# Optimization experiments

Hardware: AMD Instinct MI355X
Metric: run time of the kernel (lower is better)

The kernel has to match this reference:

```python
import jax, jax.numpy as jnp
import numpy as np

B, T, D, H = 2, 2048, 1024, 16
DH = D // H  # 64


def setup_inputs() -> dict:
    key = jax.random.key(0)
    ks = jax.random.split(key, 6)
    s = 1.0 / np.sqrt(D)
    return {
        "x": jax.random.normal(ks[0], (B, T, D), dtype=jnp.float32),
        "Wq": jax.random.normal(ks[1], (D, D), dtype=jnp.float32) * s,
        "Wk": jax.random.normal(ks[2], (D, D), dtype=jnp.float32) * s,
        "Wv": jax.random.normal(ks[3], (D, D), dtype=jnp.float32) * s,
        "Wo": jax.random.normal(ks[4], (D, D), dtype=jnp.float32) * s,
        "bo": jnp.zeros((D,), dtype=jnp.float32),
    }


def reference(x, Wq, Wk, Wv, Wo, bo):
    b, t, _ = x.shape
    # projections (torch Linear: x @ W.T; here W stored as [d_in, d_out])
    q = (x @ Wq).reshape(b, t, H, DH).transpose(0, 2, 1, 3)  # [b,H,t,dh]
    k = (x @ Wk).reshape(b, t, H, DH).transpose(0, 2, 1, 3)
    v = (x @ Wv).reshape(b, t, H, DH).transpose(0, 2, 1, 3)
    scores = jnp.einsum("bhqd,bhkd->bhqk", q, k) / np.sqrt(DH).astype(np.float32)
    causal = jnp.tril(jnp.ones((t, t), dtype=bool))  # True = keep
    scores = jnp.where(causal, scores, -jnp.inf)
    weights = jax.nn.softmax(scores, axis=-1)
    ctx = jnp.einsum("bhqk,bhkd->bhqd", weights, v)
    ctx = ctx.transpose(0, 2, 1, 3).reshape(b, t, D)
    return ctx @ Wo + bo
```

## Files before the change

kernel.cpp:

```cpp
#include <hip/hip_runtime.h>


typedef unsigned short u16;
typedef __attribute__((ext_vector_type(8))) short short8;
typedef __attribute__((ext_vector_type(4))) short short4_t;
typedef __attribute__((ext_vector_type(4))) float f32x4;

#define B_ 2
#define T_ 2048
#define D_ 1024
#define H_ 16
#define DH_ 64
#define M_ (B_ * T_)
#define SCALE_LOG2E 0.18033688011112042f
#define NEG_BIG -3.0e4f

#define SLOT_F 4160
#define SLOTS_PER_BH 72
#define OPART_BYTES ((size_t)32 * SLOTS_PER_BH * SLOT_F * 4)
#define WS_BASE_BYTES ((size_t)24 * 1024 * 1024 * 2)

#define GLOAD16(g, l)                                                     \
  __builtin_amdgcn_global_load_lds(                                       \
      (const __attribute__((address_space(1))) void*)(g),                 \
      (__attribute__((address_space(3))) void*)(l), 16, 0, 0)

__device__ __forceinline__ u16 f2bf(float f) {
  union { float f; unsigned u; } v; v.f = f;
  unsigned r = v.u + 0x7fffu + ((v.u >> 16) & 1u);
  return (u16)(r >> 16);
}
__device__ __forceinline__ u16 f2bf_trunc(float f) {
  union { float f; unsigned u; } v; v.f = f;
  return (u16)(v.u >> 16);
}
__device__ __forceinline__ float exp2_raw(float x) {
  float r;
  asm volatile("v_exp_f32 %0, %1" : "=v"(r) : "v"(x));
  return r;
}

__global__ __launch_bounds__(256) void cvt_x(const float* __restrict__ x,
                                             u16* __restrict__ xb) {
  const int i = (blockIdx.x * 256 + threadIdx.x) * 8;
  float4 a = *(const float4*)(x + i);
  float4 b = *(const float4*)(x + i + 4);
  short8 o;
  o[0] = (short)f2bf(a.x); o[1] = (short)f2bf(a.y);
  o[2] = (short)f2bf(a.z); o[3] = (short)f2bf(a.w);
  o[4] = (short)f2bf(b.x); o[5] = (short)f2bf(b.y);
  o[6] = (short)f2bf(b.z); o[7] = (short)f2bf(b.w);
  *(short8*)(xb + i) = o;
}

__global__ __launch_bounds__(256) void transpose_w(
    const float* __restrict__ w0, const float* __restrict__ w1,
    const float* __restrict__ w2, const float* __restrict__ w3,
    u16* __restrict__ outT) {
  __shared__ u16 Tl[64][72];
  const int z = blockIdx.z;
  const float* src = (z == 0) ? w0 : (z == 1) ? w1 : (z == 2) ? w2 : w3;
  const int r0 = blockIdx.y * 64, c0 = blockIdx.x * 64;
  const int tid = threadIdx.x;
  const int rr = tid >> 2, cc = (tid & 3) * 16;

  const float* p = src + (size_t)(r0 + rr) * D_ + c0 + cc;
  float4 f0 = *(const float4*)p;
  float4 f1 = *(const float4*)(p + 4);
  float4 f2 = *(const float4*)(p + 8);
  float4 f3 = *(const float4*)(p + 12);
  Tl[rr][cc + 0] = f2bf(f0.x); Tl[rr][cc + 1] = f2bf(f0.y);
  Tl[rr][cc + 2] = f2bf(f0.z); Tl[rr][cc + 3] = f2bf(f0.w);
  Tl[rr][cc + 4] = f2bf(f1.x); Tl[rr][cc + 5] = f2bf(f1.y);
  Tl[rr][cc + 6] = f2bf(f1.z); Tl[rr][cc + 7] = f2bf(f1.w);
  Tl[rr][cc + 8] = f2bf(f2.x); Tl[rr][cc + 9] = f2bf(f2.y);
  Tl[rr][cc +10] = f2bf(f2.z); Tl[rr][cc +11] = f2bf(f2.w);
  Tl[rr][cc +12] = f2bf(f3.x); Tl[rr][cc +13] = f2bf(f3.y);
  Tl[rr][cc +14] = f2bf(f3.z); Tl[rr][cc +15] = f2bf(f3.w);
  __syncthreads();

  u16* o = outT + (size_t)z * D_ * D_ + (size_t)(c0 + rr) * D_ + r0 + cc;
  short8 x0, x1;
#pragma unroll
  for (int i = 0; i < 8; i++) x0[i] = (short)Tl[cc + i][rr];
#pragma unroll
  for (int i = 0; i < 8; i++) x1[i] = (short)Tl[cc + 8 + i][rr];
  *(short8*)o = x0;
  *(short8*)(o + 8) = x1;
}

__global__ __launch_bounds__(256) void qkv_gemm(
    const u16* __restrict__ x, const u16* __restrict__ wT,
    u16* __restrict__ qkv) {
  __shared__ u16 As[128][32];
  __shared__ u16 Bs[128][32];

  const int z = blockIdx.z;
  const u16* W = wT + (size_t)z * D_ * D_;
  u16* out = qkv + (size_t)z * M_ * D_;
  const int n0 = blockIdx.x * 128;
  const int m0 = blockIdx.y * 128;
  const int tid = threadIdx.x;
  const int lane = tid & 63, w = tid >> 6;
  const int quad = lane >> 4, l16 = lane & 15;
  const int wr = w >> 1, wc = w & 1;

  f32x4 acc[4][4] = {};
  const int grow = w * 16 + (lane >> 2);
  const int gcol = (lane & 3) * 8;
  u16* lA = (u16*)As + w * 512;
  u16* lB = (u16*)Bs + w * 512;

  for (int k0 = 0; k0 < D_; k0 += 32) {
    const u16* gA = x + (size_t)(m0 + grow) * D_ + k0 + gcol;
    const u16* gB = W + (size_t)(n0 + grow) * D_ + k0 + gcol;
    GLOAD16(gA, lA);
    GLOAD16(gA + (size_t)64 * D_, lA + 2048);
    GLOAD16(gB, lB);
    GLOAD16(gB + (size_t)64 * D_, lB + 2048);
    __syncthreads();

    short8 af[4], bf[4];
#pragma unroll
    for (int i = 0; i < 4; i++)
      af[i] = *(const short8*)&As[wr * 64 + i * 16 + l16][quad * 8];
#pragma unroll
    for (int i = 0; i < 4; i++)
      bf[i] = *(const short8*)&Bs[wc * 64 + i * 16 + l16][quad * 8];
#pragma unroll
    for (int i = 0; i < 4; i++)
#pragma unroll
      for (int j = 0; j < 4; j++)
        acc[i][j] = __builtin_amdgcn_mfma_f32_16x16x32_bf16(af[i], bf[j], acc[i][j], 0, 0, 0);
    __syncthreads();
  }

  const float osc = (z == 0) ? SCALE_LOG2E : 1.0f;
#pragma unroll
  for (int i = 0; i < 4; i++) {
#pragma unroll
    for (int j = 0; j < 4; j++) {
      const int n = n0 + wc * 64 + j * 16 + l16;
      const int h = n >> 6, dh = n & 63;
#pragma unroll
      for (int r = 0; r < 4; r++) {
        const int m = m0 + wr * 64 + i * 16 + quad * 4 + r;
        const int b = m >> 11, t = m & (T_ - 1);
        out[(((size_t)(b * H_ + h)) * T_ + t) * DH_ + dh] = f2bf(acc[i][j][r] * osc);
      }
    }
  }
}

__global__ __launch_bounds__(256) void transpose_v(
    const u16* __restrict__ v, u16* __restrict__ vT) {
  __shared__ u16 Tl[64][72];
  const int t0 = blockIdx.x * 64;
  const int bh = blockIdx.y;
  const int tid = threadIdx.x;
  const int rr = tid >> 2, cc = (tid & 3) * 16;

  const u16* p = v + (size_t)bh * T_ * DH_ + (size_t)(t0 + rr) * DH_ + cc;
  short8 a0 = *(const short8*)p;
  short8 a1 = *(const short8*)(p + 8);
  *(short8*)&Tl[rr][cc] = a0;
  *(short8*)&Tl[rr][cc + 8] = a1;
  __syncthreads();

  u16* o = vT + (size_t)bh * DH_ * T_ + (size_t)rr * T_ + t0 + cc;
  short8 x0, x1;
#pragma unroll
  for (int i = 0; i < 8; i++) x0[i] = (short)Tl[cc + i][rr];
#pragma unroll
  for (int i = 0; i < 8; i++) x1[i] = (short)Tl[cc + 8 + i][rr];
  *(short8*)o = x0;
  *(short8*)(o + 8) = x1;
}

__device__ __forceinline__ int slot_base(int qt) {
  return (qt < 16) ? (qt - 8) * 2
       : (qt < 24) ? 16 + (qt - 16) * 3
                   : 40 + (qt - 24) * 4;
}

__global__ __launch_bounds__(128) void attn_chunk(
    const u16* __restrict__ qg, const u16* __restrict__ kg,
    const u16* __restrict__ vtg, u16* __restrict__ ctx,
    float* __restrict__ Opart) {
  __shared__ u16 Ks[64][72];
  __shared__ u16 Vs[64][72];
  __shared__ u16 Ps[2][2][16][72];

  const int cid = 79 - blockIdx.x;
  int qt, c, nc;
  if (cid < 8)       { qt = cid;                    c = 0;               nc = 1; }
  else if (cid < 24) { qt = 8  + ((cid - 8) >> 1);  c = (cid - 8) & 1;   nc = 2; }
  else if (cid < 48) { qt = 16 + (cid - 24) / 3;    c = (cid - 24) % 3;  nc = 3; }
  else               { qt = 24 + ((cid - 48) >> 2); c = (cid - 48) & 3;  nc = 4; }
  const int nt = qt + 1;
  const int kv_lo = (c * nt / nc) * 64;
  const int kv_hi = ((c + 1) * nt / nc) * 64;
  const int q0 = qt * 64;

  const int bh = blockIdx.y;
  const int tid = threadIdx.x;
  const int w = tid >> 6, lane = tid & 63;
  const int quad = lane >> 4, l16 = lane & 15;
  const size_t baseQK = (size_t)bh * T_ * DH_;
  const size_t baseV  = (size_t)bh * DH_ * T_;

  const int qrowA = q0 + w * 32 + l16;
  const int qrowB = qrowA + 16;
  short8 qfA0 = *(const short8*)(qg + baseQK + (size_t)qrowA * DH_ + quad * 8);
  short8 qfA1 = *(const short8*)(qg + baseQK + (size_t)qrowA * DH_ + 32 + quad * 8);
  short8 qfB0 = *(const short8*)(qg + baseQK + (size_t)qrowB * DH_ + quad * 8);
  short8 qfB1 = *(const short8*)(qg + baseQK + (size_t)qrowB * DH_ + 32 + quad * 8);

  f32x4 oaccA[4] = {}, oaccB[4] = {};
  float liA = 0.f, liB = 0.f;

  const int srow = tid >> 1;
  const int scol = (tid & 1) * 32;

  const u16* kp = kg + baseQK + (size_t)(kv_lo + srow) * DH_ + scol;
  const u16* vp = vtg + baseV + (size_t)srow * T_ + kv_lo + scol;
  short8 kr0 = *(const short8*)kp;
  short8 kr1 = *(const short8*)(kp + 8);
  short8 kr2 = *(const short8*)(kp + 16);
  short8 kr3 = *(const short8*)(kp + 24);
  short8 vr0 = *(const short8*)vp;
  short8 vr1 = *(const short8*)(vp + 8);
  short8 vr2 = *(const short8*)(vp + 16);
  short8 vr3 = *(const short8*)(vp + 24);

  for (int kv0 = kv_lo; kv0 < kv_hi; kv0 += 64) {
    __syncthreads();
    *(short8*)&Ks[srow][scol]      = kr0;
    *(short8*)&Ks[srow][scol + 8]  = kr1;
    *(short8*)&Ks[srow][scol + 16] = kr2;
    *(short8*)&Ks[srow][scol + 24] = kr3;
    *(short8*)&Vs[srow][scol]      = vr0;
    *(short8*)&Vs[srow][scol + 8]  = vr1;
    *(short8*)&Vs[srow][scol + 16] = vr2;
    *(short8*)&Vs[srow][scol + 24] = vr3;
    if (kv0 + 64 < kv_hi) {
      const u16* kn = kg + baseQK + (size_t)(kv0 + 64 + srow) * DH_ + scol;
      const u16* vn = vtg + baseV + (size_t)srow * T_ + kv0 + 64 + scol;
      kr0 = *(const short8*)kn;
      kr1 = *(const short8*)(kn + 8);
      kr2 = *(const short8*)(kn + 16);
      kr3 = *(const short8*)(kn + 24);
      vr0 = *(const short8*)vn;
      vr1 = *(const short8*)(vn + 8);
      vr2 = *(const short8*)(vn + 16);
      vr3 = *(const short8*)(vn + 24);
    }
    __syncthreads();

    short8 kf0[4], kf1[4];
#pragma unroll
    for (int cb = 0; cb < 4; cb++) {
      kf0[cb] = *(const short8*)&Ks[cb * 16 + l16][quad * 8];
      kf1[cb] = *(const short8*)&Ks[cb * 16 + l16][32 + quad * 8];
    }

    f32x4 svA[4], svB[4];
    __builtin_amdgcn_s_setprio(1);
#pragma unroll
    for (int cb = 0; cb < 4; cb++) {
      f32x4 z = {};
      svA[cb] = __builtin_amdgcn_mfma_f32_16x16x32_bf16(kf0[cb], qfA0, z, 0, 0, 0);
      svA[cb] = __builtin_amdgcn_mfma_f32_16x16x32_bf16(kf1[cb], qfA1, svA[cb], 0, 0, 0);
      svB[cb] = __builtin_amdgcn_mfma_f32_16x16x32_bf16(kf0[cb], qfB0, z, 0, 0, 0);
      svB[cb] = __builtin_amdgcn_mfma_f32_16x16x32_bf16(kf1[cb], qfB1, svB[cb], 0, 0, 0);
    }
    __builtin_amdgcn_s_setprio(0);

    float pA[4][4], pB[4][4];
    if (kv0 == q0) {
#pragma unroll
      for (int cb = 0; cb < 4; cb++)
#pragma unroll
        for (int r = 0; r < 4; r++) {
          const int kv = kv0 + cb * 16 + quad * 4 + r;
          pA[cb][r] = exp2_raw((kv <= qrowA) ? svA[cb][r] : NEG_BIG);
          pB[cb][r] = exp2_raw((kv <= qrowB) ? svB[cb][r] : NEG_BIG);
        }
    } else {
#pragma unroll
      for (int cb = 0; cb < 4; cb++)
#pragma unroll
        for (int r = 0; r < 4; r++) {
          pA[cb][r] = exp2_raw(svA[cb][r]);
          pB[cb][r] = exp2_raw(svB[cb][r]);
        }
    }
#pragma unroll
    for (int cb = 0; cb < 4; cb++)
#pragma unroll
      for (int r = 0; r < 4; r++) { liA += pA[cb][r]; liB += pB[cb][r]; }

    short8 vf0[4], vf1[4];
#pragma unroll
    for (int cb = 0; cb < 4; cb++) {
      vf0[cb] = *(const short8*)&Vs[cb * 16 + l16][quad * 8];
      vf1[cb] = *(const short8*)&Vs[cb * 16 + l16][32 + quad * 8];
    }

#pragma unroll
    for (int cb = 0; cb < 4; cb++) {
      short4_t pkA, pkB;
#pragma unroll
      for (int r = 0; r < 4; r++) {
        pkA[r] = (short)f2bf_trunc(pA[cb][r]);
        pkB[r] = (short)f2bf_trunc(pB[cb][r]);
      }
      *(short4_t*)&Ps[w][0][l16][cb * 16 + quad * 4] = pkA;
      *(short4_t*)&Ps[w][1][l16][cb * 16 + quad * 4] = pkB;
    }
    short8 paA0 = *(const short8*)&Ps[w][0][l16][quad * 8];
    short8 paA1 = *(const short8*)&Ps[w][0][l16][32 + quad * 8];
    short8 paB0 = *(const short8*)&Ps[w][1][l16][quad * 8];
    short8 paB1 = *(const short8*)&Ps[w][1][l16][32 + quad * 8];
    __builtin_amdgcn_s_setprio(1);
#pragma unroll
    for (int cb = 0; cb < 4; cb++) {
      oaccA[cb] = __builtin_amdgcn_mfma_f32_16x16x32_bf16(vf0[cb], paA0, oaccA[cb], 0, 0, 0);
      oaccA[cb] = __builtin_amdgcn_mfma_f32_16x16x32_bf16(vf1[cb], paA1, oaccA[cb], 0, 0, 0);
      oaccB[cb] = __builtin_amdgcn_mfma_f32_16x16x32_bf16(vf0[cb], paB0, oaccB[cb], 0, 0, 0);
      oaccB[cb] = __builtin_amdgcn_mfma_f32_16x16x32_bf16(vf1[cb], paB1, oaccB[cb], 0, 0, 0);
    }
    __builtin_amdgcn_s_setprio(0);
  }

  liA += __shfl_xor(liA, 16, 64); liA += __shfl_xor(liA, 32, 64);
  liB += __shfl_xor(liB, 16, 64); liB += __shfl_xor(liB, 32, 64);

  if (nc == 1) {
    const int b = bh >> 4, h = bh & 15;
    const float invA = 1.0f / liA, invB = 1.0f / liB;
    u16* outA = ctx + ((size_t)(b * T_ + qrowA)) * D_ + h * 64 + quad * 4;
    u16* outB = ctx + ((size_t)(b * T_ + qrowB)) * D_ + h * 64 + quad * 4;
#pragma unroll
    for (int cb = 0; cb < 4; cb++) {
      short4_t oA, oB;
#pragma unroll
      for (int r = 0; r < 4; r++) {
        oA[r] = (short)f2bf(oaccA[cb][r] * invA);
        oB[r] = (short)f2bf(oaccB[cb][r] * invB);
      }
      *(short4_t*)(outA + cb * 16) = oA;
      *(short4_t*)(outB + cb * 16) = oB;
    }
  } else {
    float* slot = Opart + ((size_t)bh * SLOTS_PER_BH + slot_base(qt) + c) * SLOT_F;
    float* pA = slot + (size_t)(w * 32 + l16) * 64 + quad * 4;
    float* pB = slot + (size_t)(w * 32 + 16 + l16) * 64 + quad * 4;
#pragma unroll
    for (int cb = 0; cb < 4; cb++) {
      *(f32x4*)(pA + cb * 16) = oaccA[cb];
      *(f32x4*)(pB + cb * 16) = oaccB[cb];
    }
    if (quad == 0) {
      slot[4096 + w * 32 + l16] = liA;
      slot[4096 + w * 32 + 16 + l16] = liB;
    }
  }
}

__global__ __launch_bounds__(256) void attn_combine(
    const float* __restrict__ Opart, u16* __restrict__ ctx) {
  __shared__ float ls[64];
  const int qt = blockIdx.x + 8;
  const int bh = blockIdx.y;
  const int nc = 1 + (qt >> 3);
  const float* slot0 = Opart + ((size_t)bh * SLOTS_PER_BH + slot_base(qt)) * SLOT_F;
  const int tid = threadIdx.x;

  if (tid < 64) {
    float s = 0.f;
    for (int c = 0; c < nc; c++) s += slot0[(size_t)c * SLOT_F + 4096 + tid];
    ls[tid] = 1.0f / s;
  }
  __syncthreads();

  const int q = tid >> 2, d0 = (tid & 3) * 16;
  const float* p = slot0 + (size_t)q * 64 + d0;
  f32x4 a0 = *(const f32x4*)(p);
  f32x4 a1 = *(const f32x4*)(p + 4);
  f32x4 a2 = *(const f32x4*)(p + 8);
  f32x4 a3 = *(const f32x4*)(p + 12);
  for (int c = 1; c < nc; c++) {
    const float* pc = p + (size_t)c * SLOT_F;
    a0 += *(const f32x4*)(pc);
    a1 += *(const f32x4*)(pc + 4);
    a2 += *(const f32x4*)(pc + 8);
    a3 += *(const f32x4*)(pc + 12);
  }
  const float inv = ls[q];
  short8 o0, o1;
#pragma unroll
  for (int i = 0; i < 4; i++) {
    o0[i]     = (short)f2bf(a0[i] * inv);
    o0[i + 4] = (short)f2bf(a1[i] * inv);
    o1[i]     = (short)f2bf(a2[i] * inv);
    o1[i + 4] = (short)f2bf(a3[i] * inv);
  }
  const int b = bh >> 4, h = bh & 15;
  u16* op = ctx + ((size_t)(b * T_ + qt * 64 + q)) * D_ + h * 64 + d0;
  *(short8*)op = o0;
  *(short8*)(op + 8) = o1;
}

__global__ __launch_bounds__(128) void attn_mono(
    const u16* __restrict__ qg, const u16* __restrict__ kg,
    const u16* __restrict__ vtg, u16* __restrict__ ctx) {
  __shared__ u16 Ks[64][72];
  __shared__ u16 Vs[64][72];
  __shared__ u16 Ps[2][2][16][72];

  const int qt = gridDim.x - 1 - blockIdx.x;
  const int bh = blockIdx.y;
  const int tid = threadIdx.x;
  const int w = tid >> 6, lane = tid & 63;
  const int quad = lane >> 4, l16 = lane & 15;
  const int q0 = qt * 64;
  const size_t baseQK = (size_t)bh * T_ * DH_;
  const size_t baseV  = (size_t)bh * DH_ * T_;

  const int qrowA = q0 + w * 32 + l16;
  const int qrowB = qrowA + 16;
  short8 qfA0 = *(const short8*)(qg + baseQK + (size_t)qrowA * DH_ + quad * 8);
  short8 qfA1 = *(const short8*)(qg + baseQK + (size_t)qrowA * DH_ + 32 + quad * 8);
  short8 qfB0 = *(const short8*)(qg + baseQK + (size_t)qrowB * DH_ + quad * 8);
  short8 qfB1 = *(const short8*)(qg + baseQK + (size_t)qrowB * DH_ + 32 + quad * 8);

  f32x4 oaccA[4] = {}, oaccB[4] = {};
  float liA = 0.f, liB = 0.f;

  const int srow = tid >> 1;
  const int scol = (tid & 1) * 32;

  const u16* kp = kg + baseQK + (size_t)srow * DH_ + scol;
  const u16* vp = vtg + baseV + (size_t)srow * T_ + scol;
  short8 kr0 = *(const short8*)kp;
  short8 kr1 = *(const short8*)(kp + 8);
  short8 kr2 = *(const short8*)(kp + 16);
  short8 kr3 = *(const short8*)(kp + 24);
  short8 vr0 = *(const short8*)vp;
  short8 vr1 = *(const short8*)(vp + 8);
  short8 vr2 = *(const short8*)(vp + 16);
  short8 vr3 = *(const short8*)(vp + 24);

  for (int kv0 = 0; kv0 <= q0; kv0 += 64) {
    __syncthreads();
    *(short8*)&Ks[srow][scol]      = kr0;
    *(short8*)&Ks[srow][scol + 8]  = kr1;
    *(short8*)&Ks[srow][scol + 16] = kr2;
    *(short8*)&Ks[srow][scol + 24] = kr3;
    *(short8*)&Vs[srow][scol]      = vr0;
    *(short8*)&Vs[srow][scol + 8]  = vr1;
    *(short8*)&Vs[srow][scol + 16] = vr2;
    *(short8*)&Vs[srow][scol + 24] = vr3;
    if (kv0 < q0) {
      const u16* kn = kg + baseQK + (size_t)(kv0 + 64 + srow) * DH_ + scol;
      const u16* vn = vtg + baseV + (size_t)srow * T_ + kv0 + 64 + scol;
      kr0 = *(const short8*)kn;
      kr1 = *(const short8*)(kn + 8);
      kr2 = *(const short8*)(kn + 16);
      kr3 = *(const short8*)(kn + 24);
      vr0 = *(const short8*)vn;
      vr1 = *(const short8*)(vn + 8);
      vr2 = *(const short8*)(vn + 16);
      vr3 = *(const short8*)(vn + 24);
    }
    __syncthreads();

    short8 kf0[4], kf1[4];
#pragma unroll
    for (int cb = 0; cb < 4; cb++) {
      kf0[cb] = *(const short8*)&Ks[cb * 16 + l16][quad * 8];
      kf1[cb] = *(const short8*)&Ks[cb * 16 + l16][32 + quad * 8];
    }

    f32x4 svA[4], svB[4];
#pragma unroll
    for (int cb = 0; cb < 4; cb++) {
      f32x4 z = {};
      svA[cb] = __builtin_amdgcn_mfma_f32_16x16x32_bf16(kf0[cb], qfA0, z, 0, 0, 0);
      svA[cb] = __builtin_amdgcn_mfma_f32_16x16x32_bf16(kf1[cb], qfA1, svA[cb], 0, 0, 0);
      svB[cb] = __builtin_amdgcn_mfma_f32_16x16x32_bf16(kf0[cb], qfB0, z, 0, 0, 0);
      svB[cb] = __builtin_amdgcn_mfma_f32_16x16x32_bf16(kf1[cb], qfB1, svB[cb], 0, 0, 0);
    }

    float pA[4][4], pB[4][4];
    if (kv0 == q0) {
#pragma unroll
      for (int cb = 0; cb < 4; cb++)
#pragma unroll
        for (int r = 0; r < 4; r++) {
          const int kv = kv0 + cb * 16 + quad * 4 + r;
          pA[cb][r] = exp2_raw((kv <= qrowA) ? svA[cb][r] : NEG_BIG);
          pB[cb][r] = exp2_raw((kv <= qrowB) ? svB[cb][r] : NEG_BIG);
        }
    } else {
#pragma unroll
      for (int cb = 0; cb < 4; cb++)
#pragma unroll
        for (int r = 0; r < 4; r++) {
          pA[cb][r] = exp2_raw(svA[cb][r]);
          pB[cb][r] = exp2_raw(svB[cb][r]);
        }
    }
#pragma unroll
    for (int cb = 0; cb < 4; cb++)
#pragma unroll
      for (int r = 0; r < 4; r++) { liA += pA[cb][r]; liB += pB[cb][r]; }

    short8 vf0[4], vf1[4];
#pragma unroll
    for (int cb = 0; cb < 4; cb++) {
      vf0[cb] = *(const short8*)&Vs[cb * 16 + l16][quad * 8];
      vf1[cb] = *(const short8*)&Vs[cb * 16 + l16][32 + quad * 8];
    }

#pragma unroll
    for (int cb = 0; cb < 4; cb++) {
      short4_t pkA, pkB;
#pragma unroll
      for (int r = 0; r < 4; r++) {
        pkA[r] = (short)f2bf_trunc(pA[cb][r]);
        pkB[r] = (short)f2bf_trunc(pB[cb][r]);
      }
      *(short4_t*)&Ps[w][0][l16][cb * 16 + quad * 4] = pkA;
      *(short4_t*)&Ps[w][1][l16][cb * 16 + quad * 4] = pkB;
    }
    short8 paA0 = *(const short8*)&Ps[w][0][l16][quad * 8];
    short8 paA1 = *(const short8*)&Ps[w][0][l16][32 + quad * 8];
    short8 paB0 = *(const short8*)&Ps[w][1][l16][quad * 8];
    short8 paB1 = *(const short8*)&Ps[w][1][l16][32 + quad * 8];
#pragma unroll
    for (int cb = 0; cb < 4; cb++) {
      oaccA[cb] = __builtin_amdgcn_mfma_f32_16x16x32_bf16(vf0[cb], paA0, oaccA[cb], 0, 0, 0);
      oaccA[cb] = __builtin_amdgcn_mfma_f32_16x16x32_bf16(vf1[cb], paA1, oaccA[cb], 0, 0, 0);
      oaccB[cb] = __builtin_amdgcn_mfma_f32_16x16x32_bf16(vf0[cb], paB0, oaccB[cb], 0, 0, 0);
      oaccB[cb] = __builtin_amdgcn_mfma_f32_16x16x32_bf16(vf1[cb], paB1, oaccB[cb], 0, 0, 0);
    }
  }

  liA += __shfl_xor(liA, 16, 64); liA += __shfl_xor(liA, 32, 64);
  liB += __shfl_xor(liB, 16, 64); liB += __shfl_xor(liB, 32, 64);
  const int b = bh >> 4, h = bh & 15;
  const float invA = 1.0f / liA, invB = 1.0f / liB;
  u16* outA = ctx + ((size_t)(b * T_ + qrowA)) * D_ + h * 64 + quad * 4;
  u16* outB = ctx + ((size_t)(b * T_ + qrowB)) * D_ + h * 64 + quad * 4;
#pragma unroll
  for (int cb = 0; cb < 4; cb++) {
    short4_t oA, oB;
#pragma unroll
    for (int r = 0; r < 4; r++) {
      oA[r] = (short)f2bf(oaccA[cb][r] * invA);
      oB[r] = (short)f2bf(oaccB[cb][r] * invB);
    }
    *(short4_t*)(outA + cb * 16) = oA;
    *(short4_t*)(outB + cb * 16) = oB;
  }
}

__global__ __launch_bounds__(256) void out_gemm(
    const u16* __restrict__ ctx, const u16* __restrict__ woT,
    const float* __restrict__ bo, float* __restrict__ out) {
  __shared__ u16 As[64][32];
  __shared__ u16 Bs[128][32];

  const int n0 = blockIdx.x * 128;
  const int m0 = blockIdx.y * 64;
  const int tid = threadIdx.x;
  const int lane = tid & 63, w = tid >> 6;
  const int quad = lane >> 4, l16 = lane & 15;
  const int wr = w >> 1, wc = w & 1;

  f32x4 acc[2][4] = {};
  const int grow = w * 16 + (lane >> 2);
  const int gcol = (lane & 3) * 8;
  u16* lA = (u16*)As + w * 512;
  u16* lB = (u16*)Bs + w * 512;

  for (int k0 = 0; k0 < D_; k0 += 32) {
    const u16* gA = ctx + (size_t)(m0 + grow) * D_ + k0 + gcol;
    const u16* gB = woT + (size_t)(n0 + grow) * D_ + k0 + gcol;
    GLOAD16(gA, lA);
    GLOAD16(gB, lB);
    GLOAD16(gB + (size_t)64 * D_, lB + 2048);
    __syncthreads();

    short8 af[2], bf[4];
#pragma unroll
    for (int i = 0; i < 2; i++)
      af[i] = *(const short8*)&As[wr * 32 + i * 16 + l16][quad * 8];
#pragma unroll
    for (int i = 0; i < 4; i++)
      bf[i] = *(const short8*)&Bs[wc * 64 + i * 16 + l16][quad * 8];
#pragma unroll
    for (int i = 0; i < 2; i++)
#pragma unroll
      for (int j = 0; j < 4; j++)
        acc[i][j] = __builtin_amdgcn_mfma_f32_16x16x32_bf16(af[i], bf[j], acc[i][j], 0, 0, 0);
    __syncthreads();
  }

#pragma unroll
  for (int i = 0; i < 2; i++) {
#pragma unroll
    for (int j = 0; j < 4; j++) {
      const int n = n0 + wc * 64 + j * 16 + l16;
      const float bias = bo[n];
#pragma unroll
      for (int r = 0; r < 4; r++) {
        const int m = m0 + wr * 32 + i * 16 + quad * 4 + r;
        out[(size_t)m * D_ + n] = acc[i][j][r] + bias;
      }
    }
  }
}

extern "C" void kernel_launch(void* const* d_in, const int* in_sizes, int n_in,
                              void* d_out, int out_size, void* d_ws, size_t ws_size,
                              hipStream_t stream) {
  const float* x  = (const float*)d_in[0];
  const float* Wq = (const float*)d_in[1];
  const float* Wk = (const float*)d_in[2];
  const float* Wv = (const float*)d_in[3];
  const float* Wo = (const float*)d_in[4];
  const float* bo = (const float*)d_in[5];
  float* out = (float*)d_out;

  u16* ws  = (u16*)d_ws;
  u16* xb  = ws;
  u16* wT  = xb + (size_t)M_ * D_;
  u16* qkv = wT + (size_t)4 * D_ * D_;
  u16* ctx = qkv + (size_t)3 * M_ * D_;
  u16* vT  = xb;
  float* Opart = (float*)(ctx + (size_t)M_ * D_);

  cvt_x<<<dim3(M_ * D_ / (256 * 8)), 256, 0, stream>>>(x, xb);
  transpose_w<<<dim3(16, 16, 4), 256, 0, stream>>>(Wq, Wk, Wv, Wo, wT);
  qkv_gemm<<<dim3(D_ / 128, M_ / 128, 3), 256, 0, stream>>>(xb, wT, qkv);
  transpose_v<<<dim3(T_ / 64, B_ * H_), 256, 0, stream>>>(qkv + (size_t)2 * M_ * D_, vT);

  if (ws_size >= WS_BASE_BYTES + OPART_BYTES) {
    attn_chunk<<<dim3(80, B_ * H_), 128, 0, stream>>>(
        qkv, qkv + (size_t)M_ * D_, vT, ctx, Opart);
    attn_combine<<<dim3(24, B_ * H_), 256, 0, stream>>>(Opart, ctx);
  } else {
    attn_mono<<<dim3(T_ / 64, B_ * H_), 128, 0, stream>>>(
        qkv, qkv + (size_t)M_ * D_, vT, ctx);
  }

  out_gemm<<<dim3(D_ / 128, M_ / 64), 256, 0, stream>>>(ctx, wT + (size_t)3 * D_ * D_, bo, out);
}
```

Before: 198.1 us.

## Load K/V MFMA fragments directly from global memory, dropping LDS staging

The attention kernel no longer stages K and V tiles in shared memory behind two barriers per iteration. Each wave now loads its MFMA operand fragments straight from global memory (served by L2/L1, since both waves read the same data), and the launch bounds request 4 blocks per SIMD. This removes the LDS write/read traffic and the block-wide syncs, and the lower LDS footprint may allow more blocks per CU. The cost is duplicated global loads across the two waves and no register prefetch of the next tile, so latency is exposed unless occupancy hides it.

```diff
diff --git a/kernel.cpp b/kernel.cpp
--- a/kernel.cpp
+++ b/kernel.cpp
@@ -183,12 +183,10 @@
                    : 40 + (qt - 24) * 4;
 }
 
-__global__ __launch_bounds__(128) void attn_chunk(
+__global__ __launch_bounds__(128, 4) void attn_chunk(
     const u16* __restrict__ qg, const u16* __restrict__ kg,
     const u16* __restrict__ vtg, u16* __restrict__ ctx,
     float* __restrict__ Opart) {
-  __shared__ u16 Ks[64][72];
-  __shared__ u16 Vs[64][72];
   __shared__ u16 Ps[2][2][16][72];
 
   const int cid = 79 - blockIdx.x;
@@ -219,49 +217,22 @@
   f32x4 oaccA[4] = {}, oaccB[4] = {};
   float liA = 0.f, liB = 0.f;
 
-  const int srow = tid >> 1;
-  const int scol = (tid & 1) * 32;
-
-  const u16* kp = kg + baseQK + (size_t)(kv_lo + srow) * DH_ + scol;
-  const u16* vp = vtg + baseV + (size_t)srow * T_ + kv_lo + scol;
-  short8 kr0 = *(const short8*)kp;
-  short8 kr1 = *(const short8*)(kp + 8);
-  short8 kr2 = *(const short8*)(kp + 16);
-  short8 kr3 = *(const short8*)(kp + 24);
-  short8 vr0 = *(const short8*)vp;
-  short8 vr1 = *(const short8*)(vp + 8);
-  short8 vr2 = *(const short8*)(vp + 16);
-  short8 vr3 = *(const short8*)(vp + 24);
+  const u16* kRow = kg + baseQK + (size_t)l16 * DH_ + quad * 8;
+  const u16* vRow = vtg + baseV + (size_t)l16 * T_ + quad * 8;
 
   for (int kv0 = kv_lo; kv0 < kv_hi; kv0 += 64) {
-    __syncthreads();
-    *(short8*)&Ks[srow][scol]      = kr0;
-    *(short8*)&Ks[srow][scol + 8]  = kr1;
-    *(short8*)&Ks[srow][scol + 16] = kr2;
-    *(short8*)&Ks[srow][scol + 24] = kr3;
-    *(short8*)&Vs[srow][scol]      = vr0;
-    *(short8*)&Vs[srow][scol + 8]  = vr1;
-    *(short8*)&Vs[srow][scol + 16] = vr2;
-    *(short8*)&Vs[srow][scol + 24] = vr3;
-    if (kv0 + 64 < kv_hi) {
-      const u16* kn = kg + baseQK + (size_t)(kv0 + 64 + srow) * DH_ + scol;
-      const u16* vn = vtg + baseV + (size_t)srow * T_ + kv0 + 64 + scol;
-      kr0 = *(const short8*)kn;
-      kr1 = *(const short8*)(kn + 8);
-      kr2 = *(const short8*)(kn + 16);
-      kr3 = *(const short8*)(kn + 24);
-      vr0 = *(const short8*)vn;
-      vr1 = *(const short8*)(vn + 8);
-      vr2 = *(const short8*)(vn + 16);
-      vr3 = *(const short8*)(vn + 24);
-    }
-    __syncthreads();
-
-    short8 kf0[4], kf1[4];
-#pragma unroll
-    for (int cb = 0; cb < 4; cb++) {
-      kf0[cb] = *(const short8*)&Ks[cb * 16 + l16][quad * 8];
-      kf1[cb] = *(const short8*)&Ks[cb * 16 + l16][32 + quad * 8];
+    short8 kf0[4], kf1[4], vf0[4], vf1[4];
+#pragma unroll
+    for (int cb = 0; cb < 4; cb++) {
+      const u16* kp = kRow + (size_t)(kv0 + cb * 16) * DH_;
+      kf0[cb] = *(const short8*)kp;
+      kf1[cb] = *(const short8*)(kp + 32);
+    }
+#pragma unroll
+    for (int cb = 0; cb < 4; cb++) {
+      const u16* vp = vRow + (size_t)(cb * 16) * T_ + kv0;
+      vf0[cb] = *(const short8*)vp;
+      vf1[cb] = *(const short8*)(vp + 32);
     }
 
     f32x4 svA[4], svB[4];
@@ -299,13 +270,6 @@
     for (int cb = 0; cb < 4; cb++)
 #pragma unroll
       for (int r = 0; r < 4; r++) { liA += pA[cb][r]; liB += pB[cb][r]; }
-
-    short8 vf0[4], vf1[4];
-#pragma unroll
-    for (int cb = 0; cb < 4; cb++) {
-      vf0[cb] = *(const short8*)&Vs[cb * 16 + l16][quad * 8];
-      vf1[cb] = *(const short8*)&Vs[cb * 16 + l16][32 + quad * 8];
-    }
 
 #pragma unroll
     for (int cb = 0; cb < 4; cb++) {
```

After: 281.8 us. 42.3% more time.

## Widen attention chunk query tile to 128 rows with four waves per block

Applied to the files above, without the earlier changes.

Each attention chunk block now covers a 128-row query tile using four waves (256 threads) instead of 64 rows with two waves. Every K/V tile loaded into LDS is therefore reused by twice as many query rows, which halves K/V global traffic and the number of blocks, and the KV split table, slot layout and combine kernel are resized to match. The causal mask now applies per wave whenever a KV tile overlaps that wave's rows. In exchange the grid has half as many blocks (1280), so there is less parallelism and coarser load balancing, and some waves compute fully masked tiles on the diagonal.

```diff
diff --git a/kernel.cpp b/kernel.cpp
--- a/kernel.cpp
+++ b/kernel.cpp
@@ -15,8 +15,8 @@
 #define SCALE_LOG2E 0.18033688011112042f
 #define NEG_BIG -3.0e4f
 
-#define SLOT_F 4160
-#define SLOTS_PER_BH 72
+#define SLOT_F 8320
+#define SLOTS_PER_BH 36
 #define OPART_BYTES ((size_t)32 * SLOTS_PER_BH * SLOT_F * 4)
 #define WS_BASE_BYTES ((size_t)24 * 1024 * 1024 * 2)
 
@@ -178,29 +178,29 @@
 }
 
 __device__ __forceinline__ int slot_base(int qt) {
-  return (qt < 16) ? (qt - 8) * 2
-       : (qt < 24) ? 16 + (qt - 16) * 3
-                   : 40 + (qt - 24) * 4;
-}
-
-__global__ __launch_bounds__(128) void attn_chunk(
+  return (qt < 8)  ? (qt - 4) * 2
+       : (qt < 12) ? 8 + (qt - 8) * 3
+                   : 20 + (qt - 12) * 4;
+}
+
+__global__ __launch_bounds__(256) void attn_chunk(
     const u16* __restrict__ qg, const u16* __restrict__ kg,
     const u16* __restrict__ vtg, u16* __restrict__ ctx,
     float* __restrict__ Opart) {
   __shared__ u16 Ks[64][72];
   __shared__ u16 Vs[64][72];
-  __shared__ u16 Ps[2][2][16][72];
-
-  const int cid = 79 - blockIdx.x;
+  __shared__ u16 Ps[4][2][16][72];
+
+  const int cid = 39 - blockIdx.x;
   int qt, c, nc;
-  if (cid < 8)       { qt = cid;                    c = 0;               nc = 1; }
-  else if (cid < 24) { qt = 8  + ((cid - 8) >> 1);  c = (cid - 8) & 1;   nc = 2; }
-  else if (cid < 48) { qt = 16 + (cid - 24) / 3;    c = (cid - 24) % 3;  nc = 3; }
-  else               { qt = 24 + ((cid - 48) >> 2); c = (cid - 48) & 3;  nc = 4; }
-  const int nt = qt + 1;
+  if (cid < 4)       { qt = cid;                    c = 0;               nc = 1; }
+  else if (cid < 12) { qt = 4  + ((cid - 4) >> 1);  c = (cid - 4) & 1;   nc = 2; }
+  else if (cid < 24) { qt = 8  + (cid - 12) / 3;    c = (cid - 12) % 3;  nc = 3; }
+  else               { qt = 12 + ((cid - 24) >> 2); c = (cid - 24) & 3;  nc = 4; }
+  const int nt = 2 * (qt + 1);
   const int kv_lo = (c * nt / nc) * 64;
   const int kv_hi = ((c + 1) * nt / nc) * 64;
-  const int q0 = qt * 64;
+  const int q0 = qt * 128;
 
   const int bh = blockIdx.y;
   const int tid = threadIdx.x;
@@ -209,7 +209,8 @@
   const size_t baseQK = (size_t)bh * T_ * DH_;
   const size_t baseV  = (size_t)bh * DH_ * T_;
 
-  const int qrowA = q0 + w * 32 + l16;
+  const int qw0 = q0 + w * 32;
+  const int qrowA = qw0 + l16;
   const int qrowB = qrowA + 16;
   short8 qfA0 = *(const short8*)(qg + baseQK + (size_t)qrowA * DH_ + quad * 8);
   short8 qfA1 = *(const short8*)(qg + baseQK + (size_t)qrowA * DH_ + 32 + quad * 8);
@@ -219,41 +220,29 @@
   f32x4 oaccA[4] = {}, oaccB[4] = {};
   float liA = 0.f, liB = 0.f;
 
-  const int srow = tid >> 1;
-  const int scol = (tid & 1) * 32;
+  const int srow = tid >> 2;
+  const int scol = (tid & 3) * 16;
 
   const u16* kp = kg + baseQK + (size_t)(kv_lo + srow) * DH_ + scol;
   const u16* vp = vtg + baseV + (size_t)srow * T_ + kv_lo + scol;
   short8 kr0 = *(const short8*)kp;
   short8 kr1 = *(const short8*)(kp + 8);
-  short8 kr2 = *(const short8*)(kp + 16);
-  short8 kr3 = *(const short8*)(kp + 24);
   short8 vr0 = *(const short8*)vp;
   short8 vr1 = *(const short8*)(vp + 8);
-  short8 vr2 = *(const short8*)(vp + 16);
-  short8 vr3 = *(const short8*)(vp + 24);
 
   for (int kv0 = kv_lo; kv0 < kv_hi; kv0 += 64) {
     __syncthreads();
-    *(short8*)&Ks[srow][scol]      = kr0;
-    *(short8*)&Ks[srow][scol + 8]  = kr1;
-    *(short8*)&Ks[srow][scol + 16] = kr2;
-    *(short8*)&Ks[srow][scol + 24] = kr3;
-    *(short8*)&Vs[srow][scol]      = vr0;
-    *(short8*)&Vs[srow][scol + 8]  = vr1;
-    *(short8*)&Vs[srow][scol + 16] = vr2;
-    *(short8*)&Vs[srow][scol + 24] = vr3;
+    *(short8*)&Ks[srow][scol]     = kr0;
+    *(short8*)&Ks[srow][scol + 8] = kr1;
+    *(short8*)&Vs[srow][scol]     = vr0;
+    *(short8*)&Vs[srow][scol + 8] = vr1;
     if (kv0 + 64 < kv_hi) {
       const u16* kn = kg + baseQK + (size_t)(kv0 + 64 + srow) * DH_ + scol;
       const u16* vn = vtg + baseV + (size_t)srow * T_ + kv0 + 64 + scol;
       kr0 = *(const short8*)kn;
       kr1 = *(const short8*)(kn + 8);
-      kr2 = *(const short8*)(kn + 16);
-      kr3 = *(const short8*)(kn + 24);
       vr0 = *(const short8*)vn;
       vr1 = *(const short8*)(vn + 8);
-      vr2 = *(const short8*)(vn + 16);
-      vr3 = *(const short8*)(vn + 24);
     }
     __syncthreads();
 
@@ -277,7 +266,7 @@
     __builtin_amdgcn_s_setprio(0);
 
     float pA[4][4], pB[4][4];
-    if (kv0 == q0) {
+    if (kv0 + 63 > qw0) {
 #pragma unroll
       for (int cb = 0; cb < 4; cb++)
 #pragma unroll
@@ -362,54 +351,68 @@
       *(f32x4*)(pB + cb * 16) = oaccB[cb];
     }
     if (quad == 0) {
-      slot[4096 + w * 32 + l16] = liA;
-      slot[4096 + w * 32 + 16 + l16] = liB;
+      slot[8192 + w * 32 + l16] = liA;
+      slot[8192 + w * 32 + 16 + l16] = liB;
     }
   }
 }
 
 __global__ __launch_bounds__(256) void attn_combine(
     const float* __restrict__ Opart, u16* __restrict__ ctx) {
-  __shared__ float ls[64];
-  const int qt = blockIdx.x + 8;
+  __shared__ float ls[128];
+  const int qt = blockIdx.x + 4;
   const int bh = blockIdx.y;
-  const int nc = 1 + (qt >> 3);
+  const int nc = 1 + (qt >> 2);
   const float* slot0 = Opart + ((size_t)bh * SLOTS_PER_BH + slot_base(qt)) * SLOT_F;
   const int tid = threadIdx.x;
 
-  if (tid < 64) {
+  if (tid < 128) {
     float s = 0.f;
-    for (int c = 0; c < nc; c++) s += slot0[(size_t)c * SLOT_F + 4096 + tid];
+    for (int c = 0; c < nc; c++) s += slot0[(size_t)c * SLOT_F + 8192 + tid];
     ls[tid] = 1.0f / s;
   }
   __syncthreads();
 
-  const int q = tid >> 2, d0 = (tid & 3) * 16;
+  const int q = tid >> 1, d0 = (tid & 1) * 32;
   const float* p = slot0 + (size_t)q * 64 + d0;
   f32x4 a0 = *(const f32x4*)(p);
   f32x4 a1 = *(const f32x4*)(p + 4);
   f32x4 a2 = *(const f32x4*)(p + 8);
   f32x4 a3 = *(const f32x4*)(p + 12);
+  f32x4 a4 = *(const f32x4*)(p + 16);
+  f32x4 a5 = *(const f32x4*)(p + 20);
+  f32x4 a6 = *(const f32x4*)(p + 24);
+  f32x4 a7 = *(const f32x4*)(p + 28);
   for (int c = 1; c < nc; c++) {
     const float* pc = p + (size_t)c * SLOT_F;
     a0 += *(const f32x4*)(pc);
     a1 += *(const f32x4*)(pc + 4);
     a2 += *(const f32x4*)(pc + 8);
     a3 += *(const f32x4*)(pc + 12);
+    a4 += *(const f32x4*)(pc + 16);
+    a5 += *(const f32x4*)(pc + 20);
+    a6 += *(const f32x4*)(pc + 24);
+    a7 += *(const f32x4*)(pc + 28);
   }
   const float inv = ls[q];
-  short8 o0, o1;
+  short8 o0, o1, o2, o3;
 #pragma unroll
   for (int i = 0; i < 4; i++) {
     o0[i]     = (short)f2bf(a0[i] * inv);
     o0[i + 4] = (short)f2bf(a1[i] * inv);
     o1[i]     = (short)f2bf(a2[i] * inv);
     o1[i + 4] = (short)f2bf(a3[i] * inv);
+    o2[i]     = (short)f2bf(a4[i] * inv);
+    o2[i + 4] = (short)f2bf(a5[i] * inv);
+    o3[i]     = (short)f2bf(a6[i] * inv);
+    o3[i + 4] = (short)f2bf(a7[i] * inv);
   }
   const int b = bh >> 4, h = bh & 15;
-  u16* op = ctx + ((size_t)(b * T_ + qt * 64 + q)) * D_ + h * 64 + d0;
+  u16* op = ctx + ((size_t)(b * T_ + qt * 128 + q)) * D_ + h * 64 + d0;
   *(short8*)op = o0;
   *(short8*)(op + 8) = o1;
+  *(short8*)(op + 16) = o2;
+  *(short8*)(op + 24) = o3;
 }
 
 __global__ __launch_bounds__(128) void attn_mono(
@@ -649,9 +652,9 @@
   transpose_v<<<dim3(T_ / 64, B_ * H_), 256, 0, stream>>>(qkv + (size_t)2 * M_ * D_, vT);
 
   if (ws_size >= WS_BASE_BYTES + OPART_BYTES) {
-    attn_chunk<<<dim3(80, B_ * H_), 128, 0, stream>>>(
+    attn_chunk<<<dim3(40, B_ * H_), 256, 0, stream>>>(
         qkv, qkv + (size_t)M_ * D_, vT, ctx, Opart);
-    attn_combine<<<dim3(24, B_ * H_), 256, 0, stream>>>(Opart, ctx);
+    attn_combine<<<dim3(12, B_ * H_), 256, 0, stream>>>(Opart, ctx);
   } else {
     attn_mono<<<dim3(T_ / 64, B_ * H_), 128, 0, stream>>>(
         qkv, qkv + (size_t)M_ * D_, vT, ctx);
```

Result: no change. 198.6 us (+0.2%).
